# Optimization experiments

Measured on AMD Instinct MI355X. Metric: run time of the kernel, lower is better.

## Reference

```python
import jax, jax.numpy as jnp
import numpy as np
import math

B, S, D, H, L, DFF = 64, 512, 512, 8, 2, 1024
DK = D // H
NEG = -1e32
LN_EPS = 1e-5


def cosine_pos_emb(seqlen, d_model):
    # pe[:,0::2]=sin(pos*div), pe[:,1::2]=cos(pos*div) -- fully overwrites the randn init
    pos = jnp.arange(seqlen, dtype=jnp.float32)[:, None]
    div = jnp.exp(jnp.arange(0, d_model, 2, dtype=jnp.float32) * (-math.log(10000.0) / d_model))
    ang = pos * div  # [S, D/2]
    return jnp.stack([jnp.sin(ang), jnp.cos(ang)], axis=-1).reshape(seqlen, d_model)


def layernorm(x, g, b):
    m = jnp.mean(x, axis=-1, keepdims=True)
    v = jnp.var(x, axis=-1, keepdims=True)
    return g * (x - m) * jax.lax.rsqrt(v + LN_EPS) + b


def setup_inputs() -> dict:
    key = jax.random.key(0)
    ks = jax.random.split(key, 8)
    sc = 0.02
    inp = {
        'q_embed_data': jax.random.normal(ks[0], (B, S, D), jnp.float32),
        'qa_embed_data': jax.random.normal(ks[1], (B, S, D), jnp.float32),
        'forget_rate': jax.random.uniform(ks[2], (B, 1, S, 1), jnp.float32),
        # per-block params, leading dim = n_blocks (kq_same=1: q uses k_linear)
        'Wk': jax.random.normal(ks[3], (L, D, D), jnp.float32) * sc,
        'bk': jnp.zeros((L, D), jnp.float32),
        'Wv': jax.random.normal(ks[4], (L, D, D), jnp.float32) * sc,
        'bv': jnp.zeros((L, D), jnp.float32),
        'Wo': jax.random.normal(ks[5], (L, D, D), jnp.float32) * sc,
        'bo': jnp.zeros((L, D), jnp.float32),
        'ln1_g': jnp.ones((L, D), jnp.float32),
        'ln1_b': jnp.zeros((L, D), jnp.float32),
        'W1': jax.random.normal(ks[6], (L, D, DFF), jnp.float32) * sc,
        'b1': jnp.zeros((L, DFF), jnp.float32),
        'W2': jax.random.normal(ks[7], (L, DFF, D), jnp.float32) * sc,
        'b2': jnp.zeros((L, D), jnp.float32),
        'ln2_g': jnp.ones((L, D), jnp.float32),
        'ln2_b': jnp.zeros((L, D), jnp.float32),
    }
    return inp


def reference(q_embed_data, qa_embed_data, forget_rate, Wk, bk, Wv, bv, Wo, bo,
              ln1_g, ln1_b, W1, b1, W2, b2, ln2_g, ln2_b):
    pe = cosine_pos_emb(S, D)
    x = q_embed_data + pe  # query/key stream
    y = qa_embed_data + pe  # value stream (fixed across blocks)
    # mask=0 path: np.triu(ones, k=0) == 0 -> strictly lower-triangular allowed
    allow = jnp.tril(jnp.ones((S, S), dtype=bool), -1)
    scale = 1.0 / math.sqrt(DK)
    for i in range(L):
        qk = (x @ Wk[i] + bk[i]).reshape(B, S, H, DK).transpose(0, 2, 1, 3)  # [B,H,S,dk]
        v = (y @ Wv[i] + bv[i]).reshape(B, S, H, DK).transpose(0, 2, 1, 3)
        scores = jnp.einsum('bhqd,bhkd->bhqk', qk, qk) * scale
        scores = scores * forget_rate  # [B,1,S,1] broadcasts over heads and keys
        scores = jnp.where(allow, scores, NEG)
        p = jax.nn.softmax(scores, axis=-1)
        p = p.at[:, :, 0, :].set(0.0)  # zero_pad: first query row zeroed
        attn = jnp.einsum('bhqk,bhkd->bhqd', p, v).transpose(0, 2, 1, 3).reshape(B, S, D)
        attn = attn @ Wo[i] + bo[i]
        x = layernorm(x + attn, ln1_g[i], ln1_b[i])
        ff = jax.nn.relu(x @ W1[i] + b1[i]) @ W2[i] + b2[i]
        x = layernorm(x + ff, ln2_g[i], ln2_b[i])
    return x
```

## Files before the change

kernel.cpp:

```cpp
#include <hip/hip_runtime.h>
#include <cstdio>

#define B_   64
#define S_   512
#define D_   512
#define H_   8
#define DK_  64
#define DFF_ 1024
#define L_   2
#define BS_  (B_ * S_)

typedef __attribute__((ext_vector_type(8))) short bf16x8;
typedef __attribute__((ext_vector_type(4))) short bf16x4;
typedef __attribute__((ext_vector_type(4))) float f32x4;

__device__ inline short f2bf(float f) {
  unsigned u = __float_as_uint(f);
  u = u + 0x7FFF + ((u >> 16) & 1);
  return (short)(u >> 16);
}
__device__ inline float bf2f(short s) {
  return __uint_as_float(((unsigned)(unsigned short)s) << 16);
}

__device__ inline void gl_lds16(const short* g, void* lds_base) {
  __builtin_amdgcn_global_load_lds(
      (const __attribute__((address_space(1))) void*)g,
      (__attribute__((address_space(3))) void*)lds_base, 16, 0, 0);
}

__global__ void pe_kernel(float* __restrict__ pe) {
  int idx = blockIdx.x * 256 + threadIdx.x;
  int s = idx >> 9, d = idx & 511;
  float dv = __expf((float)(d & ~1) * (-9.210340371976184f / (float)D_));
  float ang = (float)s * dv;
  pe[idx] = (d & 1) ? cosf(ang) : sinf(ang);
}

__global__ __launch_bounds__(256) void prep_kernel(
    const float* __restrict__ q, const float* __restrict__ qa,
    const float* __restrict__ pe, float* __restrict__ x,
    short* __restrict__ xb, short* __restrict__ yb) {
  size_t base = ((size_t)blockIdx.x * 256 + threadIdx.x) * 8;
  int sd = (int)(base & (size_t)(S_ * D_ - 1));
  f32x4 p0 = *(const f32x4*)(pe + sd);
  f32x4 p1 = *(const f32x4*)(pe + sd + 4);
  f32x4 q0 = *(const f32x4*)(q + base);
  f32x4 q1 = *(const f32x4*)(q + base + 4);
  f32x4 a0 = *(const f32x4*)(qa + base);
  f32x4 a1 = *(const f32x4*)(qa + base + 4);
  f32x4 x0, x1; bf16x8 xv, yv;
#pragma unroll
  for (int i = 0; i < 4; ++i) {
    float xe = q0[i] + p0[i]; x0[i] = xe; xv[i] = f2bf(xe);
    yv[i] = f2bf(a0[i] + p0[i]);
  }
#pragma unroll
  for (int i = 0; i < 4; ++i) {
    float xe = q1[i] + p1[i]; x1[i] = xe; xv[4 + i] = f2bf(xe);
    yv[4 + i] = f2bf(a1[i] + p1[i]);
  }
  *(f32x4*)(x + base) = x0;
  *(f32x4*)(x + base + 4) = x1;
  *(bf16x8*)(xb + base) = xv;
  *(bf16x8*)(yb + base) = yv;
}

struct TrArgs {
  const float* src[10];
  short* dst[10];
  int R[10], C[10];
};
__global__ __launch_bounds__(256) void tr_w_all(TrArgs a) {
  const int slot = blockIdx.z;
  const int R = a.R[slot], C = a.C[slot];
  const int c0 = blockIdx.x * 64, r0 = blockIdx.y * 64;
  if (c0 >= C || r0 >= R) return;
  const float* __restrict__ src = a.src[slot];
  short* __restrict__ dst = a.dst[slot];
  __shared__ short Ts[64][72];
  const int t = threadIdx.x;
#pragma unroll
  for (int it = 0; it < 2; ++it) {
    int c2 = it * 256 + t;
    int srow = c2 >> 3, schunk = c2 & 7;
    const float* sp = src + (size_t)(r0 + srow) * C + c0 + schunk * 8;
    f32x4 a0 = *(const f32x4*)sp;
    f32x4 a1 = *(const f32x4*)(sp + 4);
#pragma unroll
    for (int k = 0; k < 4; ++k) Ts[srow][schunk * 8 + k] = f2bf(a0[k]);
#pragma unroll
    for (int k = 0; k < 4; ++k) Ts[srow][schunk * 8 + 4 + k] = f2bf(a1[k]);
  }
  __syncthreads();
#pragma unroll
  for (int it = 0; it < 2; ++it) {
    int c2 = it * 256 + t;
    int orow = c2 >> 3, ochunk = c2 & 7;
    bf16x8 vv;
#pragma unroll
    for (int k = 0; k < 8; ++k) vv[k] = Ts[ochunk * 8 + k][orow];
    *(bf16x8*)(dst + (size_t)(c0 + orow) * R + r0 + ochunk * 8) = vv;
  }
}

__global__ __launch_bounds__(256) void gemm_bt(
    const short* __restrict__ A, const short* __restrict__ BT,
    const float* __restrict__ bias, short* __restrict__ Cb,
    int M, int N, int K, int relu, int bias_row, int nx, int xmaj)
{
  const int nwg = gridDim.x;
  const int cpx = nwg >> 3;
  const int l = (blockIdx.x & 7) * cpx + (blockIdx.x >> 3);
  int bcol, brow;
  if (xmaj) { bcol = l % nx; brow = l / nx; }
  else      { int ny = nwg / nx; brow = l % ny; bcol = l / ny; }

  __shared__ __align__(16) short As[2][128][32];
  __shared__ __align__(16) short Bs[2][128][32];
  const int t = threadIdx.x;
  const int w = t >> 6, lane = t & 63, lr = lane & 15, lk = lane >> 4;
  const int wrow = w >> 1, wcol = w & 1;

  const f32x4 vzero = {0.f, 0.f, 0.f, 0.f};
  f32x4 acc[4][4];
#pragma unroll
  for (int m = 0; m < 4; ++m)
#pragma unroll
    for (int n = 0; n < 4; ++n) acc[m][n] = vzero;

  const short* Abase = A + (size_t)brow * 128 * K;
  const short* Bbase = BT + (size_t)bcol * 128 * K;

  auto stage = [&](int buf, int k0) {
#pragma unroll
    for (int it = 0; it < 2; ++it) {
      int cb = it * 256 + w * 64;
      int c = cb + lane;
      int row = c >> 2, seg = c & 3;
      gl_lds16(Abase + (size_t)row * K + k0 + seg * 8, (char*)&As[buf][0][0] + (size_t)cb * 16);
      gl_lds16(Bbase + (size_t)row * K + k0 + seg * 8, (char*)&Bs[buf][0][0] + (size_t)cb * 16);
    }
  };

  stage(0, 0);
  int cur = 0;
  for (int k0 = 0; k0 < K; k0 += 32) {
    if (k0 + 32 < K) {
      stage(cur ^ 1, k0 + 32);
      asm volatile("s_waitcnt vmcnt(4)" ::: "memory");
    } else {
      asm volatile("s_waitcnt vmcnt(0)" ::: "memory");
    }
    asm volatile("s_barrier" ::: "memory");

    bf16x8 af[4], bf[4];
#pragma unroll
    for (int m = 0; m < 4; ++m) af[m] = *(const bf16x8*)&As[cur][wrow * 64 + m * 16 + lr][lk * 8];
#pragma unroll
    for (int n = 0; n < 4; ++n) bf[n] = *(const bf16x8*)&Bs[cur][wcol * 64 + n * 16 + lr][lk * 8];
#pragma unroll
    for (int m = 0; m < 4; ++m)
#pragma unroll
      for (int n = 0; n < 4; ++n)
        acc[m][n] = __builtin_amdgcn_mfma_f32_16x16x32_bf16(bf[n], af[m], acc[m][n], 0, 0, 0);

    asm volatile("s_barrier" ::: "memory");
    cur ^= 1;
  }

#pragma unroll
  for (int m = 0; m < 4; ++m) {
    int row = brow * 128 + wrow * 64 + m * 16 + lr;
    float brv = (bias && bias_row) ? bias[row] : 0.f;
    size_t rb = (size_t)row * N;
#pragma unroll
    for (int n = 0; n < 4; ++n) {
      int colb = bcol * 128 + wcol * 64 + n * 16 + lk * 4;
      f32x4 bv4;
      if (bias && !bias_row) bv4 = *(const f32x4*)(bias + colb);
      else { bv4[0] = brv; bv4[1] = brv; bv4[2] = brv; bv4[3] = brv; }
      bf16x4 ov;
#pragma unroll
      for (int j = 0; j < 4; ++j) {
        float vv = acc[m][n][j] + bv4[j];
        if (relu) vv = fmaxf(vv, 0.f);
        ov[j] = f2bf(vv);
      }
      *(bf16x4*)(Cb + rb + colb) = ov;
    }
  }
}

template<int P>
__device__ __forceinline__ void attn_body(
    const short* __restrict__ qk, const short* __restrict__ vT,
    const float* __restrict__ fr, short* __restrict__ out,
    short (*Pl)[552], float (*redsum)[32][4],
    int h, int b, int w, int lr, int lk)
{
  constexpr int qo0 = 32 * P, qo1 = 32 * (15 - P);
  constexpr int c0 = 2 * P + 2;
  constexpr int colb1 = c0 * 16;

  const size_t qk_head = (size_t)b * S_ * D_ + (size_t)h * DK_;
  const float scale = 0.125f;

  bf16x8 qf0[2][2], qf1[2][2];
#pragma unroll
  for (int qt = 0; qt < 2; ++qt)
#pragma unroll
    for (int ks = 0; ks < 2; ++ks) {
      qf0[qt][ks] = *(const bf16x8*)(qk + qk_head + (size_t)(qo0 + qt * 16 + lr) * D_ + ks * 32 + lk * 8);
      qf1[qt][ks] = *(const bf16x8*)(qk + qk_head + (size_t)(qo1 + qt * 16 + lr) * D_ + ks * 32 + lk * 8);
    }

  float frv0[2], frv1[2];
#pragma unroll
  for (int qt = 0; qt < 2; ++qt) {
    frv0[qt] = scale * fr[(size_t)b * S_ + qo0 + qt * 16 + lr];
    frv1[qt] = scale * fr[(size_t)b * S_ + qo1 + qt * 16 + lr];
  }

  const f32x4 vzero = {0.f, 0.f, 0.f, 0.f};
  f32x4 acc[9][2];
#pragma unroll
  for (int i = 0; i < 9; ++i) { acc[i][0] = vzero; acc[i][1] = vzero; }

#pragma unroll
  for (int frag = 0; frag < 34; ++frag) {
    if ((frag & 3) == w) {
      const int i = frag >> 2;
      if (frag < c0) {
        const int kt = frag;
#pragma unroll
        for (int ks = 0; ks < 2; ++ks) {
          bf16x8 kf = *(const bf16x8*)(qk + qk_head + (size_t)(kt * 16 + lr) * D_ + ks * 32 + lk * 8);
          acc[i][0] = __builtin_amdgcn_mfma_f32_16x16x32_bf16(kf, qf0[0][ks], acc[i][0], 0, 0, 0);
          acc[i][1] = __builtin_amdgcn_mfma_f32_16x16x32_bf16(kf, qf0[1][ks], acc[i][1], 0, 0, 0);
        }
      } else {
        const int kt = frag - c0;
#pragma unroll
        for (int ks = 0; ks < 2; ++ks) {
          bf16x8 kf = *(const bf16x8*)(qk + qk_head + (size_t)(kt * 16 + lr) * D_ + ks * 32 + lk * 8);
          acc[i][0] = __builtin_amdgcn_mfma_f32_16x16x32_bf16(kf, qf1[0][ks], acc[i][0], 0, 0, 0);
          acc[i][1] = __builtin_amdgcn_mfma_f32_16x16x32_bf16(kf, qf1[1][ks], acc[i][1], 0, 0, 0);
        }
      }
    }
  }

  float rs00 = 0.f, rs01 = 0.f, rs10 = 0.f, rs11 = 0.f;
#pragma unroll
  for (int frag = 0; frag < 34; ++frag) {
    if ((frag & 3) == w) {
      const int i = frag >> 2;
      const int tl = (frag < c0) ? 0 : 1;
      const int kt = tl ? frag - c0 : frag;
      const int kbase = kt * 16 + lk * 4;
      const int colb = (tl ? colb1 : 0) + kbase;
#pragma unroll
      for (int qt = 0; qt < 2; ++qt) {
        int qrow = (tl ? qo1 : qo0) + qt * 16 + lr;
        float fv = tl ? frv1[qt] : frv0[qt];
        bf16x4 pk;
        float rs = 0.f;
#pragma unroll
        for (int j = 0; j < 4; ++j) {
          float e = (kbase + j < qrow) ? __expf(acc[i][qt][j] * fv) : 0.f;
          rs += e;
          pk[j] = f2bf(e);
        }
        *(bf16x4*)&Pl[qt * 16 + lr][colb] = pk;
        if (tl == 0) { if (qt == 0) rs00 += rs; else rs01 += rs; }
        else         { if (qt == 0) rs10 += rs; else rs11 += rs; }
      }
    }
  }

#pragma unroll
  for (int msk = 16; msk < 64; msk <<= 1) {
    rs00 += __shfl_xor(rs00, msk);
    rs01 += __shfl_xor(rs01, msk);
    rs10 += __shfl_xor(rs10, msk);
    rs11 += __shfl_xor(rs11, msk);
  }
  if (lk == 0) {
    redsum[0][lr][w] = rs00;
    redsum[0][16 + lr][w] = rs01;
    redsum[1][lr][w] = rs10;
    redsum[1][16 + lr][w] = rs11;
  }
  __syncthreads();

  const int uqt0 = w & 1, udh0 = w >> 1;
  const int uqt1 = w >> 1, udh1 = w & 1;
  f32x4 oacc0[2] = {vzero, vzero}, oacc1[2] = {vzero, vzero};

#pragma unroll
  for (int kb = 0; kb < 16; ++kb) {
    if (kb < P + 1) {
      bf16x8 pa = *(const bf16x8*)&Pl[uqt0 * 16 + lr][kb * 32 + lk * 8];
#pragma unroll
      for (int n = 0; n < 2; ++n) {
        bf16x8 vf = *(const bf16x8*)(vT + (size_t)(h * DK_ + udh0 * 32 + n * 16 + lr) * BS_
                                        + (size_t)b * S_ + kb * 32 + lk * 8);
        oacc0[n] = __builtin_amdgcn_mfma_f32_16x16x32_bf16(pa, vf, oacc0[n], 0, 0, 0);
      }
    }
    if (kb < 16 - P) {
      bf16x8 pa = *(const bf16x8*)&Pl[uqt1 * 16 + lr][colb1 + kb * 32 + lk * 8];
#pragma unroll
      for (int n = 0; n < 2; ++n) {
        bf16x8 vf = *(const bf16x8*)(vT + (size_t)(h * DK_ + udh1 * 32 + n * 16 + lr) * BS_
                                        + (size_t)b * S_ + kb * 32 + lk * 8);
        oacc1[n] = __builtin_amdgcn_mfma_f32_16x16x32_bf16(pa, vf, oacc1[n], 0, 0, 0);
      }
    }
  }

  {
    float invd[4];
#pragma unroll
    for (int j = 0; j < 4; ++j) {
      int row = uqt0 * 16 + lk * 4 + j;
      float ds = redsum[0][row][0] + redsum[0][row][1] + redsum[0][row][2] + redsum[0][row][3];
      invd[j] = ds > 0.f ? 1.f / ds : 0.f;
    }
#pragma unroll
    for (int n = 0; n < 2; ++n)
#pragma unroll
      for (int j = 0; j < 4; ++j) {
        int qrow = qo0 + uqt0 * 16 + lk * 4 + j;
        out[qk_head + (size_t)qrow * D_ + udh0 * 32 + n * 16 + lr] = f2bf(oacc0[n][j] * invd[j]);
      }
  }
  {
    float invd[4];
#pragma unroll
    for (int j = 0; j < 4; ++j) {
      int row = uqt1 * 16 + lk * 4 + j;
      float ds = redsum[1][row][0] + redsum[1][row][1] + redsum[1][row][2] + redsum[1][row][3];
      invd[j] = ds > 0.f ? 1.f / ds : 0.f;
    }
#pragma unroll
    for (int n = 0; n < 2; ++n)
#pragma unroll
      for (int j = 0; j < 4; ++j) {
        int qrow = qo1 + uqt1 * 16 + lk * 4 + j;
        out[qk_head + (size_t)qrow * D_ + udh1 * 32 + n * 16 + lr] = f2bf(oacc1[n][j] * invd[j]);
      }
  }
}

__global__ __launch_bounds__(256, 4) void attn_kernel(
    const short* __restrict__ qk, const short* __restrict__ vT,
    const float* __restrict__ fr, short* __restrict__ out)
{
  const int hw = blockIdx.x;
  const int l = (hw & 7) * 512 + (hw >> 3);
  const int p = l & 7, hb = l >> 3;
  const int h = hb & 7, b = hb >> 3;
  const int t = threadIdx.x;
  const int w = t >> 6, lr = t & 15, lk = (t & 63) >> 4;

  __shared__ short Pl[32][552];
  __shared__ float redsum[2][32][4];

  switch (p) {
    case 0: attn_body<0>(qk, vT, fr, out, Pl, redsum, h, b, w, lr, lk); break;
    case 1: attn_body<1>(qk, vT, fr, out, Pl, redsum, h, b, w, lr, lk); break;
    case 2: attn_body<2>(qk, vT, fr, out, Pl, redsum, h, b, w, lr, lk); break;
    case 3: attn_body<3>(qk, vT, fr, out, Pl, redsum, h, b, w, lr, lk); break;
    case 4: attn_body<4>(qk, vT, fr, out, Pl, redsum, h, b, w, lr, lk); break;
    case 5: attn_body<5>(qk, vT, fr, out, Pl, redsum, h, b, w, lr, lk); break;
    case 6: attn_body<6>(qk, vT, fr, out, Pl, redsum, h, b, w, lr, lk); break;
    case 7: attn_body<7>(qk, vT, fr, out, Pl, redsum, h, b, w, lr, lk); break;
  }
}

__global__ __launch_bounds__(256) void ln_res(
    const float* __restrict__ xin, const short* __restrict__ add,
    const float* __restrict__ g, const float* __restrict__ bb,
    float* __restrict__ xout, short* __restrict__ xbout)
{
  const int row = blockIdx.x * 4 + (threadIdx.x >> 6);
  const int lane = threadIdx.x & 63;
  const size_t base = (size_t)row * D_ + lane * 8;

  f32x4 a0 = *(const f32x4*)(xin + base);
  f32x4 a1 = *(const f32x4*)(xin + base + 4);
  bf16x8 av = *(const bf16x8*)(add + base);
  float vals[8];
#pragma unroll
  for (int i = 0; i < 4; ++i) vals[i] = a0[i] + bf2f(av[i]);
#pragma unroll
  for (int i = 0; i < 4; ++i) vals[4 + i] = a1[i] + bf2f(av[4 + i]);

  float s = 0.f, sq = 0.f;
#pragma unroll
  for (int i = 0; i < 8; ++i) { s += vals[i]; sq += vals[i] * vals[i]; }
#pragma unroll
  for (int m = 1; m < 64; m <<= 1) { s += __shfl_xor(s, m); sq += __shfl_xor(sq, m); }

  float mean = s * (1.f / D_);
  float var = sq * (1.f / D_) - mean * mean;
  float rstd = rsqrtf(var + 1e-5f);

  int col = lane * 8;
  f32x4 o0, o1; bf16x8 ob;
#pragma unroll
  for (int i = 0; i < 8; ++i) {
    float vv = g[col + i] * (vals[i] - mean) * rstd + bb[col + i];
    if (i < 4) o0[i] = vv; else o1[i - 4] = vv;
    ob[i] = f2bf(vv);
  }
  *(f32x4*)(xout + base) = o0;
  *(f32x4*)(xout + base + 4) = o1;
  *(bf16x8*)(xbout + base) = ob;
}

extern "C" void kernel_launch(void* const* d_in, const int* in_sizes, int n_in,
                              void* d_out, int out_size, void* d_ws, size_t ws_size,
                              hipStream_t stream) {
  const float* q_emb = (const float*)d_in[0];
  const float* qa_emb = (const float*)d_in[1];
  const float* frate = (const float*)d_in[2];
  const float* Wk = (const float*)d_in[3];
  const float* bk = (const float*)d_in[4];
  const float* Wv = (const float*)d_in[5];
  const float* bv = (const float*)d_in[6];
  const float* Wo = (const float*)d_in[7];
  const float* bo = (const float*)d_in[8];
  const float* ln1g = (const float*)d_in[9];
  const float* ln1b = (const float*)d_in[10];
  const float* W1 = (const float*)d_in[11];
  const float* b1 = (const float*)d_in[12];
  const float* W2 = (const float*)d_in[13];
  const float* b2 = (const float*)d_in[14];
  const float* ln2g = (const float*)d_in[15];
  const float* ln2b = (const float*)d_in[16];
  float* x = (float*)d_out;

  char* ws = (char*)d_ws;
  size_t off = 0;
  auto alloc = [&](size_t bytes) -> void* {
    void* p = ws + off;
    off += (bytes + 255) & ~(size_t)255;
    return p;
  };
  const size_t MTOK = (size_t)BS_;
  float* pe    = (float*)alloc((size_t)S_ * D_ * 4);
  short* xb    = (short*)alloc(MTOK * D_ * 2);
  short* yb    = (short*)alloc(MTOK * D_ * 2);
  short* qkb   = (short*)alloc(MTOK * D_ * 2);
  short* vTb   = (short*)alloc(MTOK * D_ * 2);
  short* ff1b  = (short*)alloc(MTOK * DFF_ * 2);
  short* attnb = ff1b;
  short* goutb = qkb;
  short* wT[L_][5];
  for (int i = 0; i < L_; ++i) {
    wT[i][0] = (short*)alloc((size_t)D_ * D_ * 2);
    wT[i][1] = (short*)alloc((size_t)D_ * D_ * 2);
    wT[i][2] = (short*)alloc((size_t)D_ * D_ * 2);
    wT[i][3] = (short*)alloc((size_t)D_ * DFF_ * 2);
    wT[i][4] = (short*)alloc((size_t)DFF_ * D_ * 2);
  }
  if (off > ws_size) {
    fprintf(stderr, "parKT: workspace overflow: need %zu have %zu\n", off, ws_size);
    return;
  }

  pe_kernel<<<(S_ * D_) / 256, 256, 0, stream>>>(pe);
  prep_kernel<<<(int)(MTOK * D_ / (256 * 8)), 256, 0, stream>>>(q_emb, qa_emb, pe, x, xb, yb);

  TrArgs ta;
  for (int i = 0; i < L_; ++i) {
    ta.src[i * 5 + 0] = Wk + (size_t)i * D_ * D_;  ta.dst[i * 5 + 0] = wT[i][0]; ta.R[i * 5 + 0] = D_;   ta.C[i * 5 + 0] = D_;
    ta.src[i * 5 + 1] = Wv + (size_t)i * D_ * D_;  ta.dst[i * 5 + 1] = wT[i][1]; ta.R[i * 5 + 1] = D_;   ta.C[i * 5 + 1] = D_;
    ta.src[i * 5 + 2] = Wo + (size_t)i * D_ * D_;  ta.dst[i * 5 + 2] = wT[i][2]; ta.R[i * 5 + 2] = D_;   ta.C[i * 5 + 2] = D_;
    ta.src[i * 5 + 3] = W1 + (size_t)i * D_ * DFF_; ta.dst[i * 5 + 3] = wT[i][3]; ta.R[i * 5 + 3] = D_;   ta.C[i * 5 + 3] = DFF_;
    ta.src[i * 5 + 4] = W2 + (size_t)i * DFF_ * D_; ta.dst[i * 5 + 4] = wT[i][4]; ta.R[i * 5 + 4] = DFF_; ta.C[i * 5 + 4] = D_;
  }
  tr_w_all<<<dim3(DFF_ / 64, DFF_ / 64, 10), 256, 0, stream>>>(ta);

  const int M = (int)MTOK;
  for (int i = 0; i < L_; ++i) {
    gemm_bt<<<(D_ / 128) * (M / 128), 256, 0, stream>>>(xb, wT[i][0], bk + (size_t)i * D_, qkb, M, D_, D_, 0, 0, D_ / 128, 1);
    gemm_bt<<<(M / 128) * (D_ / 128), 256, 0, stream>>>(wT[i][1], yb, bv + (size_t)i * D_, vTb, D_, M, D_, 0, 1, M / 128, 0);
    attn_kernel<<<(S_ / 64) * H_ * B_, 256, 0, stream>>>(qkb, vTb, frate, attnb);
    gemm_bt<<<(D_ / 128) * (M / 128), 256, 0, stream>>>(attnb, wT[i][2], bo + (size_t)i * D_, goutb, M, D_, D_, 0, 0, D_ / 128, 1);
    ln_res<<<M / 4, 256, 0, stream>>>(x, goutb, ln1g + (size_t)i * D_, ln1b + (size_t)i * D_, x, xb);
    gemm_bt<<<(DFF_ / 128) * (M / 128), 256, 0, stream>>>(xb, wT[i][3], b1 + (size_t)i * DFF_, ff1b, M, DFF_, D_, 1, 0, DFF_ / 128, 1);
    gemm_bt<<<(D_ / 128) * (M / 128), 256, 0, stream>>>(ff1b, wT[i][4], b2 + (size_t)i * D_, goutb, M, D_, DFF_, 0, 0, D_ / 128, 1);
    ln_res<<<M / 4, 256, 0, stream>>>(x, goutb, ln2g + (size_t)i * D_, ln2b + (size_t)i * D_, x, xb);
  }
}
```

Measured before the change: 882.5 us.

## Widen GEMM tile to 128x256 and software-prefetch K/V fragments in attention

The GEMM block tile grows from 128x128 to 128x256, so each wave holds a 4x8 accumulator grid and each A tile is reused across twice as many columns. Launch grids are resized to match and the occupancy hint is set to 2. The attention kernel now double-buffers key fragments in QK^T and P/V fragments in PV, issuing next-step loads before the current MFMAs, and lowers its occupancy hint from 4 to 3 to leave room for the extra registers. The intent is to raise arithmetic intensity and hide load latency, at the cost of more register pressure and fewer GEMM workgroups per launch.

```diff
diff --git a/kernel.cpp b/kernel.cpp
--- a/kernel.cpp
+++ b/kernel.cpp
@@ -104,7 +104,7 @@
   }
 }
 
-__global__ __launch_bounds__(256) void gemm_bt(
+__global__ __launch_bounds__(256, 2) void gemm_bt(
     const short* __restrict__ A, const short* __restrict__ BT,
     const float* __restrict__ bias, short* __restrict__ Cb,
     int M, int N, int K, int relu, int bias_row, int nx, int xmaj)
@@ -117,29 +117,33 @@
   else      { int ny = nwg / nx; brow = l % ny; bcol = l / ny; }
 
   __shared__ __align__(16) short As[2][128][32];
-  __shared__ __align__(16) short Bs[2][128][32];
+  __shared__ __align__(16) short Bs[2][256][32];
   const int t = threadIdx.x;
   const int w = t >> 6, lane = t & 63, lr = lane & 15, lk = lane >> 4;
-  const int wrow = w >> 1, wcol = w & 1;
+  const int wr = w >> 1, wc = w & 1;
 
   const f32x4 vzero = {0.f, 0.f, 0.f, 0.f};
-  f32x4 acc[4][4];
+  f32x4 acc[4][8];
 #pragma unroll
   for (int m = 0; m < 4; ++m)
 #pragma unroll
-    for (int n = 0; n < 4; ++n) acc[m][n] = vzero;
+    for (int n = 0; n < 8; ++n) acc[m][n] = vzero;
 
   const short* Abase = A + (size_t)brow * 128 * K;
-  const short* Bbase = BT + (size_t)bcol * 128 * K;
+  const short* Bbase = BT + (size_t)bcol * 256 * K;
 
   auto stage = [&](int buf, int k0) {
 #pragma unroll
     for (int it = 0; it < 2; ++it) {
       int cb = it * 256 + w * 64;
       int c = cb + lane;
-      int row = c >> 2, seg = c & 3;
-      gl_lds16(Abase + (size_t)row * K + k0 + seg * 8, (char*)&As[buf][0][0] + (size_t)cb * 16);
-      gl_lds16(Bbase + (size_t)row * K + k0 + seg * 8, (char*)&Bs[buf][0][0] + (size_t)cb * 16);
+      gl_lds16(Abase + (size_t)(c >> 2) * K + k0 + (c & 3) * 8, (char*)&As[buf][0][0] + (size_t)cb * 16);
+    }
+#pragma unroll
+    for (int it = 0; it < 4; ++it) {
+      int cb = it * 256 + w * 64;
+      int c = cb + lane;
+      gl_lds16(Bbase + (size_t)(c >> 2) * K + k0 + (c & 3) * 8, (char*)&Bs[buf][0][0] + (size_t)cb * 16);
     }
   };
 
@@ -148,21 +152,21 @@
   for (int k0 = 0; k0 < K; k0 += 32) {
     if (k0 + 32 < K) {
       stage(cur ^ 1, k0 + 32);
-      asm volatile("s_waitcnt vmcnt(4)" ::: "memory");
+      asm volatile("s_waitcnt vmcnt(6)" ::: "memory");
     } else {
       asm volatile("s_waitcnt vmcnt(0)" ::: "memory");
     }
     asm volatile("s_barrier" ::: "memory");
 
-    bf16x8 af[4], bf[4];
-#pragma unroll
-    for (int m = 0; m < 4; ++m) af[m] = *(const bf16x8*)&As[cur][wrow * 64 + m * 16 + lr][lk * 8];
-#pragma unroll
-    for (int n = 0; n < 4; ++n) bf[n] = *(const bf16x8*)&Bs[cur][wcol * 64 + n * 16 + lr][lk * 8];
+    bf16x8 af[4], bf[8];
+#pragma unroll
+    for (int m = 0; m < 4; ++m) af[m] = *(const bf16x8*)&As[cur][wr * 64 + m * 16 + lr][lk * 8];
+#pragma unroll
+    for (int n = 0; n < 8; ++n) bf[n] = *(const bf16x8*)&Bs[cur][wc * 128 + n * 16 + lr][lk * 8];
 #pragma unroll
     for (int m = 0; m < 4; ++m)
 #pragma unroll
-      for (int n = 0; n < 4; ++n)
+      for (int n = 0; n < 8; ++n)
         acc[m][n] = __builtin_amdgcn_mfma_f32_16x16x32_bf16(bf[n], af[m], acc[m][n], 0, 0, 0);
 
     asm volatile("s_barrier" ::: "memory");
@@ -171,12 +175,12 @@
 
 #pragma unroll
   for (int m = 0; m < 4; ++m) {
-    int row = brow * 128 + wrow * 64 + m * 16 + lr;
+    int row = brow * 128 + wr * 64 + m * 16 + lr;
     float brv = (bias && bias_row) ? bias[row] : 0.f;
     size_t rb = (size_t)row * N;
 #pragma unroll
-    for (int n = 0; n < 4; ++n) {
-      int colb = bcol * 128 + wcol * 64 + n * 16 + lk * 4;
+    for (int n = 0; n < 8; ++n) {
+      int colb = bcol * 256 + wc * 128 + n * 16 + lk * 4;
       f32x4 bv4;
       if (bias && !bias_row) bv4 = *(const f32x4*)(bias + colb);
       else { bv4[0] = brv; bv4[1] = brv; bv4[2] = brv; bv4[3] = brv; }
@@ -227,25 +231,39 @@
 #pragma unroll
   for (int i = 0; i < 9; ++i) { acc[i][0] = vzero; acc[i][1] = vzero; }
 
-#pragma unroll
-  for (int frag = 0; frag < 34; ++frag) {
-    if ((frag & 3) == w) {
-      const int i = frag >> 2;
-      if (frag < c0) {
-        const int kt = frag;
+  const int nfr = (w < 2) ? 9 : 8;
+  const short* kqbase = qk + qk_head + (size_t)lr * D_ + lk * 8;
+  auto kfoff = [&](int i) -> size_t {
+    int f = w + 4 * i;
+    int kt = (f < c0) ? f : f - c0;
+    return (size_t)kt * 16 * D_;
+  };
+  bf16x8 kbuf[2][2];
+  {
+    const short* p = kqbase + kfoff(0);
+    kbuf[0][0] = *(const bf16x8*)p;
+    kbuf[0][1] = *(const bf16x8*)(p + 32);
+  }
+#pragma unroll
+  for (int i = 0; i < 9; ++i) {
+    if (i < nfr) {
+      if (i + 1 < nfr) {
+        const short* p = kqbase + kfoff(i + 1);
+        kbuf[(i + 1) & 1][0] = *(const bf16x8*)p;
+        kbuf[(i + 1) & 1][1] = *(const bf16x8*)(p + 32);
+      }
+      const int f = w + 4 * i;
+      if (f < c0) {
 #pragma unroll
         for (int ks = 0; ks < 2; ++ks) {
-          bf16x8 kf = *(const bf16x8*)(qk + qk_head + (size_t)(kt * 16 + lr) * D_ + ks * 32 + lk * 8);
-          acc[i][0] = __builtin_amdgcn_mfma_f32_16x16x32_bf16(kf, qf0[0][ks], acc[i][0], 0, 0, 0);
-          acc[i][1] = __builtin_amdgcn_mfma_f32_16x16x32_bf16(kf, qf0[1][ks], acc[i][1], 0, 0, 0);
+          acc[i][0] = __builtin_amdgcn_mfma_f32_16x16x32_bf16(kbuf[i & 1][ks], qf0[0][ks], acc[i][0], 0, 0, 0);
+          acc[i][1] = __builtin_amdgcn_mfma_f32_16x16x32_bf16(kbuf[i & 1][ks], qf0[1][ks], acc[i][1], 0, 0, 0);
         }
       } else {
-        const int kt = frag - c0;
 #pragma unroll
         for (int ks = 0; ks < 2; ++ks) {
-          bf16x8 kf = *(const bf16x8*)(qk + qk_head + (size_t)(kt * 16 + lr) * D_ + ks * 32 + lk * 8);
-          acc[i][0] = __builtin_amdgcn_mfma_f32_16x16x32_bf16(kf, qf1[0][ks], acc[i][0], 0, 0, 0);
-          acc[i][1] = __builtin_amdgcn_mfma_f32_16x16x32_bf16(kf, qf1[1][ks], acc[i][1], 0, 0, 0);
+          acc[i][0] = __builtin_amdgcn_mfma_f32_16x16x32_bf16(kbuf[i & 1][ks], qf1[0][ks], acc[i][0], 0, 0, 0);
+          acc[i][1] = __builtin_amdgcn_mfma_f32_16x16x32_bf16(kbuf[i & 1][ks], qf1[1][ks], acc[i][1], 0, 0, 0);
         }
       }
     }
@@ -296,27 +314,45 @@
 
   const int uqt0 = w & 1, udh0 = w >> 1;
   const int uqt1 = w >> 1, udh1 = w & 1;
+  const short* vu0 = vT + (size_t)(h * DK_ + udh0 * 32 + lr) * BS_ + (size_t)b * S_ + lk * 8;
+  const short* vu1 = vT + (size_t)(h * DK_ + udh1 * 32 + lr) * BS_ + (size_t)b * S_ + lk * 8;
+  const short* prow0 = &Pl[uqt0 * 16 + lr][lk * 8];
+  const short* prow1 = &Pl[uqt1 * 16 + lr][colb1 + lk * 8];
+
   f32x4 oacc0[2] = {vzero, vzero}, oacc1[2] = {vzero, vzero};
-
+  bf16x8 paB[2][2];
+  bf16x8 vfB[2][2][2];
+  paB[0][0] = *(const bf16x8*)prow0;
+  paB[0][1] = *(const bf16x8*)prow1;
+#pragma unroll
+  for (int n = 0; n < 2; ++n) {
+    vfB[0][0][n] = *(const bf16x8*)(vu0 + (size_t)n * 16 * BS_);
+    vfB[0][1][n] = *(const bf16x8*)(vu1 + (size_t)n * 16 * BS_);
+  }
 #pragma unroll
   for (int kb = 0; kb < 16; ++kb) {
+    const int pc = kb & 1, pn = (kb + 1) & 1;
+    if (kb + 1 < P + 1) {
+      paB[pn][0] = *(const bf16x8*)(prow0 + (kb + 1) * 32);
+#pragma unroll
+      for (int n = 0; n < 2; ++n)
+        vfB[pn][0][n] = *(const bf16x8*)(vu0 + (size_t)n * 16 * BS_ + (kb + 1) * 32);
+    }
+    if (kb + 1 < 16 - P) {
+      paB[pn][1] = *(const bf16x8*)(prow1 + (kb + 1) * 32);
+#pragma unroll
+      for (int n = 0; n < 2; ++n)
+        vfB[pn][1][n] = *(const bf16x8*)(vu1 + (size_t)n * 16 * BS_ + (kb + 1) * 32);
+    }
     if (kb < P + 1) {
-      bf16x8 pa = *(const bf16x8*)&Pl[uqt0 * 16 + lr][kb * 32 + lk * 8];
-#pragma unroll
-      for (int n = 0; n < 2; ++n) {
-        bf16x8 vf = *(const bf16x8*)(vT + (size_t)(h * DK_ + udh0 * 32 + n * 16 + lr) * BS_
-                                        + (size_t)b * S_ + kb * 32 + lk * 8);
-        oacc0[n] = __builtin_amdgcn_mfma_f32_16x16x32_bf16(pa, vf, oacc0[n], 0, 0, 0);
-      }
+#pragma unroll
+      for (int n = 0; n < 2; ++n)
+        oacc0[n] = __builtin_amdgcn_mfma_f32_16x16x32_bf16(paB[pc][0], vfB[pc][0][n], oacc0[n], 0, 0, 0);
     }
     if (kb < 16 - P) {
-      bf16x8 pa = *(const bf16x8*)&Pl[uqt1 * 16 + lr][colb1 + kb * 32 + lk * 8];
-#pragma unroll
-      for (int n = 0; n < 2; ++n) {
-        bf16x8 vf = *(const bf16x8*)(vT + (size_t)(h * DK_ + udh1 * 32 + n * 16 + lr) * BS_
-                                        + (size_t)b * S_ + kb * 32 + lk * 8);
-        oacc1[n] = __builtin_amdgcn_mfma_f32_16x16x32_bf16(pa, vf, oacc1[n], 0, 0, 0);
-      }
+#pragma unroll
+      for (int n = 0; n < 2; ++n)
+        oacc1[n] = __builtin_amdgcn_mfma_f32_16x16x32_bf16(paB[pc][1], vfB[pc][1][n], oacc1[n], 0, 0, 0);
     }
   }
 
@@ -354,7 +390,7 @@
   }
 }
 
-__global__ __launch_bounds__(256, 4) void attn_kernel(
+__global__ __launch_bounds__(256, 3) void attn_kernel(
     const short* __restrict__ qk, const short* __restrict__ vT,
     const float* __restrict__ fr, short* __restrict__ out)
 {
@@ -487,13 +523,13 @@
 
   const int M = (int)MTOK;
   for (int i = 0; i < L_; ++i) {
-    gemm_bt<<<(D_ / 128) * (M / 128), 256, 0, stream>>>(xb, wT[i][0], bk + (size_t)i * D_, qkb, M, D_, D_, 0, 0, D_ / 128, 1);
-    gemm_bt<<<(M / 128) * (D_ / 128), 256, 0, stream>>>(wT[i][1], yb, bv + (size_t)i * D_, vTb, D_, M, D_, 0, 1, M / 128, 0);
+    gemm_bt<<<(M / 128) * (D_ / 256), 256, 0, stream>>>(xb, wT[i][0], bk + (size_t)i * D_, qkb, M, D_, D_, 0, 0, D_ / 256, 1);
+    gemm_bt<<<(D_ / 128) * (M / 256), 256, 0, stream>>>(wT[i][1], yb, bv + (size_t)i * D_, vTb, D_, M, D_, 0, 1, M / 256, 0);
     attn_kernel<<<(S_ / 64) * H_ * B_, 256, 0, stream>>>(qkb, vTb, frate, attnb);
-    gemm_bt<<<(D_ / 128) * (M / 128), 256, 0, stream>>>(attnb, wT[i][2], bo + (size_t)i * D_, goutb, M, D_, D_, 0, 0, D_ / 128, 1);
+    gemm_bt<<<(M / 128) * (D_ / 256), 256, 0, stream>>>(attnb, wT[i][2], bo + (size_t)i * D_, goutb, M, D_, D_, 0, 0, D_ / 256, 1);
     ln_res<<<M / 4, 256, 0, stream>>>(x, goutb, ln1g + (size_t)i * D_, ln1b + (size_t)i * D_, x, xb);
-    gemm_bt<<<(DFF_ / 128) * (M / 128), 256, 0, stream>>>(xb, wT[i][3], b1 + (size_t)i * DFF_, ff1b, M, DFF_, D_, 1, 0, DFF_ / 128, 1);
-    gemm_bt<<<(D_ / 128) * (M / 128), 256, 0, stream>>>(ff1b, wT[i][4], b2 + (size_t)i * D_, goutb, M, D_, DFF_, 0, 0, D_ / 128, 1);
+    gemm_bt<<<(M / 128) * (DFF_ / 256), 256, 0, stream>>>(xb, wT[i][3], b1 + (size_t)i * DFF_, ff1b, M, DFF_, D_, 1, 0, DFF_ / 256, 1);
+    gemm_bt<<<(M / 128) * (D_ / 256), 256, 0, stream>>>(ff1b, wT[i][4], b2 + (size_t)i * D_, goutb, M, D_, DFF_, 0, 0, D_ / 256, 1);
     ln_res<<<M / 4, 256, 0, stream>>>(x, goutb, ln2g + (size_t)i * D_, ln2b + (size_t)i * D_, x, xb);
   }
 }
```

Result: faster. 815.2 us (-7.6%).
